# Performance work log

Hardware: AMD Instinct MI355X
Metric: run time of the kernel (lower is better)

## Reference

```python
import jax, jax.numpy as jnp
import numpy as np
from jax import lax

B, C, H, W = 16, 3, 64, 64
P = 256        # total_patches
PS = 9         # patch_size
E = 256        # attn_embed_dim
NH = 8         # attn_heads
POSD = 64      # pos_embed_dim
HW = H * W
DH = E // NH


def setup_inputs() -> dict:
    key = jax.random.key(0)
    ks = jax.random.split(key, 20)
    def rn(k, shape, fan_in):
        return jax.random.normal(k, shape, jnp.float32) * (1.0 / np.sqrt(fan_in))
    return {
        "x": jax.random.normal(ks[0], (B, C, H, W), jnp.float32),
        "conv_w": rn(ks[1], (P, C, PS, PS), C * PS * PS),
        "conv_b": jnp.zeros((P,), jnp.float32),
        "in_w": rn(ks[2], (HW, E), HW),
        "in_b": jnp.zeros((E,), jnp.float32),
        "wq": rn(ks[3], (E, E), E), "bq": jnp.zeros((E,), jnp.float32),
        "wk": rn(ks[4], (E, E), E), "bk": jnp.zeros((E,), jnp.float32),
        "wv": rn(ks[5], (E, E), E), "bv": jnp.zeros((E,), jnp.float32),
        "wo": rn(ks[6], (E, E), E), "bo": jnp.zeros((E,), jnp.float32),
        "out_w": rn(ks[7], (E, HW), E),
        "out_b": jnp.zeros((HW,), jnp.float32),
        "fc_w": rn(ks[8], (HW, 2), HW),
        "fc_b": jnp.zeros((2,), jnp.float32),
        "pos_w": rn(ks[9], (2, POSD), 2),
        "pos_b": jnp.zeros((POSD,), jnp.float32),
    }


# pixel-center normalized coords matching affine_grid(align_corners=False)
_BASE = (2.0 * jnp.arange(PS, dtype=jnp.float32) + 1.0) / PS - 1.0


def _sample_patch(img, tx, ty):
    # img: (C,H,W); tx, ty scalars. Replicates affine_grid + grid_sample
    # (bilinear, padding_mode='border', align_corners=False) WITHOUT the
    # full-image repeat of the original module.
    gx = (PS / W) * _BASE[None, :] + tx     # (PS,PS) x-coords
    gy = (PS / H) * _BASE[:, None] + ty     # (PS,PS) y-coords
    ix = ((gx + 1.0) * W - 1.0) * 0.5       # unnormalize, align_corners=False
    iy = ((gy + 1.0) * H - 1.0) * 0.5
    x0 = jnp.floor(ix); y0 = jnp.floor(iy)
    wx = ix - x0;       wy = iy - y0
    x0i = jnp.clip(x0.astype(jnp.int32), 0, W - 1)
    x1i = jnp.clip(x0.astype(jnp.int32) + 1, 0, W - 1)
    y0i = jnp.clip(y0.astype(jnp.int32), 0, H - 1)
    y1i = jnp.clip(y0.astype(jnp.int32) + 1, 0, H - 1)
    v00 = img[:, y0i, x0i]; v01 = img[:, y0i, x1i]
    v10 = img[:, y1i, x0i]; v11 = img[:, y1i, x1i]
    return (v00 * (1 - wx) * (1 - wy) + v01 * wx * (1 - wy)
            + v10 * (1 - wx) * wy + v11 * wx * wy)   # (C,PS,PS)


def _forward(x, conv_w, conv_b, in_w, in_b, wq, bq, wk, bk, wv, bv, wo, bo,
             out_w, out_b, fc_w, fc_b, pos_w, pos_b):
    # ConvBlock: conv (same padding for odd kernel) + ReLU
    feat = lax.conv_general_dilated(
        x, conv_w, (1, 1), [(PS // 2, PS // 2)] * 2,
        dimension_numbers=("NCHW", "OIHW", "NCHW"))
    feat = jax.nn.relu(feat + conv_b[None, :, None, None])   # (B,P,H,W)
    # ConvSelfAttn: tokens are the P channels, features are flattened HxW
    tok = feat.reshape(B, P, HW) @ in_w + in_b                # (B,P,E)
    q = (tok @ wq + bq).reshape(B, P, NH, DH)
    k = (tok @ wk + bk).reshape(B, P, NH, DH)
    v = (tok @ wv + bv).reshape(B, P, NH, DH)
    scores = jnp.einsum("bqhd,bkhd->bhqk", q, k) / np.sqrt(DH)
    attn = jax.nn.softmax(scores, axis=-1)
    o = jnp.einsum("bhqk,bkhd->bqhd", attn, v).reshape(B, P, E)
    o = o @ wo + bo
    feat2 = o @ out_w + out_b                                 # (B,P,HW)
    # translation params in [-1,1]
    tp = jnp.tanh(feat2 @ fc_w + fc_b)                        # (B,P,2)
    tx, ty = tp[..., 0], tp[..., 1]
    sample_bp = jax.vmap(jax.vmap(_sample_patch, in_axes=(None, 0, 0)),
                         in_axes=(0, 0, 0))
    patches = sample_bp(x, tx, ty)                            # (B,P,C,PS,PS)
    patches = patches.reshape(B, P, C * PS * PS)
    pos_embeds = tp @ pos_w + pos_b                           # (B,P,POSD)
    return patches, pos_embeds


def reference(x, conv_w, conv_b, in_w, in_b, wq, bq, wk, bk, wv, bv, wo, bo,
              out_w, out_b, fc_w, fc_b, pos_w, pos_b):
    return _forward(x, conv_w, conv_b, in_w, in_b, wq, bq, wk, bk, wv, bv,
                    wo, bo, out_w, out_b, fc_w, fc_b, pos_w, pos_b)
```

## Files before the change

### kernel.cpp

```cpp
#include <hip/hip_runtime.h>
#include <hip/hip_bf16.h>

#define Bd 16
#define Cd 3
#define Hd 64
#define Wd 64
#define Pd 256
#define PSd 9
#define Ed 256
#define NHd 8
#define DHd 32
#define HWd 4096
#define POSDd 64

typedef unsigned short u16;
typedef short short8 __attribute__((ext_vector_type(8)));
typedef float f32x4 __attribute__((ext_vector_type(4)));

__device__ __forceinline__ float bf2f(u16 u) {
    union { unsigned int i; float f; } c; c.i = ((unsigned int)u) << 16; return c.f;
}
__device__ __forceinline__ u16 f2bf(float f) {
    unsigned int x = __float_as_uint(f);
    unsigned int r = (x + 0x7fffu + ((x >> 16) & 1u)) >> 16;
    return (u16)r;
}

__global__ __launch_bounds__(64) void precompute_G(
    const float* __restrict__ out_w, const float* __restrict__ fc_w,
    const float* __restrict__ out_b, const float* __restrict__ fc_b,
    float* __restrict__ G, float* __restrict__ h0) {
    int blk = blockIdx.x, lane = threadIdx.x;
    if (blk < 256) {
        int e = blk;
        float a0 = 0.f, a1 = 0.f;
        for (int i = lane; i < HWd; i += 64) {
            float a = out_w[e * HWd + i];
            a0 += a * fc_w[2 * i];
            a1 += a * fc_w[2 * i + 1];
        }
        #pragma unroll
        for (int off = 32; off; off >>= 1) { a0 += __shfl_xor(a0, off); a1 += __shfl_xor(a1, off); }
        if (lane == 0) { G[2 * e] = a0; G[2 * e + 1] = a1; }
    } else {
        int j = blk - 256;
        float a = 0.f;
        for (int i = lane; i < HWd; i += 64) a += out_b[i] * fc_w[2 * i + j];
        #pragma unroll
        for (int off = 32; off; off >>= 1) a += __shfl_xor(a, off);
        if (lane == 0) h0[j] = a + fc_b[j];
    }
}

__global__ __launch_bounds__(64) void precompute_M2(
    const float* __restrict__ wo, const float* __restrict__ bo,
    const float* __restrict__ G, float* __restrict__ M2, float* __restrict__ h0) {
    int blk = blockIdx.x, lane = threadIdx.x;
    if (blk < 256) {
        float m0 = 0.f, m1 = 0.f;
        for (int f = lane; f < Ed; f += 64) {
            float wv = wo[blk * Ed + f];
            m0 += wv * G[2 * f];
            m1 += wv * G[2 * f + 1];
        }
        #pragma unroll
        for (int off = 32; off; off >>= 1) { m0 += __shfl_xor(m0, off); m1 += __shfl_xor(m1, off); }
        if (lane == 0) { M2[2 * blk] = m0; M2[2 * blk + 1] = m1; }
    } else {
        int j = blk - 256;
        float hh = 0.f;
        for (int f = lane; f < Ed; f += 64) hh += bo[f] * G[2 * f + j];
        #pragma unroll
        for (int off = 32; off; off >>= 1) hh += __shfl_xor(hh, off);
        if (lane == 0) h0[j] += hh;
    }
}

__global__ __launch_bounds__(256) void prep_weight_t(
    const float* __restrict__ W, u16* __restrict__ Th, u16* __restrict__ Tl,
    int K, int N) {
    __shared__ u16 th[64][65];
    __shared__ u16 tl[64][65];
    int k0 = blockIdx.x * 64, n0 = blockIdx.y * 64;
    int col = threadIdx.x & 63, r4 = threadIdx.x >> 6;
    #pragma unroll
    for (int i = 0; i < 16; i++) {
        int kr = 4 * i + r4;
        float v = W[(size_t)(k0 + kr) * N + n0 + col];
        u16 h = f2bf(v);
        th[col][kr] = h;
        tl[col][kr] = f2bf(v - bf2f(h));
    }
    __syncthreads();
    #pragma unroll
    for (int i = 0; i < 16; i++) {
        int nr = 4 * i + r4;
        Th[(size_t)(n0 + nr) * K + k0 + col] = th[nr][col];
        Tl[(size_t)(n0 + nr) * K + k0 + col] = tl[nr][col];
    }
}

__global__ __launch_bounds__(256) void prep_convw(
    const float* __restrict__ W, u16* __restrict__ Ah, u16* __restrict__ Al) {
    int p = blockIdx.x, k = threadIdx.x;
    float v = (k < 243) ? W[p * 243 + k] : 0.f;
    u16 h = f2bf(v);
    Ah[p * 256 + k] = h;
    Al[p * 256 + k] = f2bf(v - bf2f(h));
}

__global__ __launch_bounds__(256) void concat_bias(
    const float* __restrict__ bq, const float* __restrict__ bk,
    const float* __restrict__ bv, float* __restrict__ b3) {
    int t = threadIdx.x;
    b3[t] = bq[t]; b3[256 + t] = bk[t]; b3[512 + t] = bv[t];
}

__global__ __launch_bounds__(256, 2) void conv_gemm(
    const u16* __restrict__ Ah, const u16* __restrict__ Al,
    const float* __restrict__ x, const float* __restrict__ conv_b,
    u16* __restrict__ feat_hi, u16* __restrict__ feat_lo) {
    __shared__ u16 sBh[64 * 72], sBl[64 * 72];
    __shared__ float wls[3 * 9 * 72];
    int tid = threadIdx.x;
    int w = tid >> 6, L = tid & 63;
    int m16 = L & 15, qd = L >> 4;
    int y = blockIdx.x;
    int nb = y << 6;
    int b = blockIdx.y;

    for (int i = tid; i < 3 * 9 * 72; i += 256) wls[i] = 0.f;
    __syncthreads();
    for (int i = tid; i < 3 * 9 * 64; i += 256) {
        int c = i / 576, rem = i - c * 576, wr = rem >> 6, col = rem & 63;
        int iy = y - 4 + wr;
        if (iy >= 0 && iy < 64)
            wls[c * 648 + wr * 72 + 4 + col] = x[((b * 3 + c) << 12) + (iy << 6) + col];
    }
    __syncthreads();

    f32x4 acc[4][4];
    #pragma unroll
    for (int mt = 0; mt < 4; mt++)
        #pragma unroll
        for (int ct = 0; ct < 4; ct++) acc[mt][ct] = (f32x4){0.f, 0.f, 0.f, 0.f};

    int n = tid >> 2, kb = (tid & 3) << 4;
    int arow = w * 16 + m16;

    for (int k0 = 0; k0 < 256; k0 += 64) {
        short8 afh[4][2], afl[4][2];
        #pragma unroll
        for (int mt = 0; mt < 4; mt++)
            #pragma unroll
            for (int c = 0; c < 2; c++) {
                int ao = (mt * 64 + arow) * 256 + k0 + c * 32 + qd * 8;
                afh[mt][c] = *(const short8*)(Ah + ao);
                afl[mt][c] = *(const short8*)(Al + ao);
            }
        u16 hbuf[16] __attribute__((aligned(8)));
        u16 lbuf[16] __attribute__((aligned(8)));
        #pragma unroll
        for (int j = 0; j < 16; j++) {
            int k = k0 + kb + j;
            float v = 0.f;
            if (k < 243) {
                int c = (k >= 81) + (k >= 162);
                int rem = k - c * 81;
                int dy = (rem * 57) >> 9;
                int dx = rem - dy * 9;
                v = wls[c * 648 + dy * 72 + dx + n];
            }
            u16 h = f2bf(v);
            hbuf[j] = h;
            lbuf[j] = f2bf(v - bf2f(h));
        }
        __syncthreads();
        #pragma unroll
        for (int t = 0; t < 4; t++) {
            *(ushort4*)&sBh[n * 72 + kb + 4 * t] = *(ushort4*)&hbuf[4 * t];
            *(ushort4*)&sBl[n * 72 + kb + 4 * t] = *(ushort4*)&lbuf[4 * t];
        }
        __syncthreads();
        #pragma unroll
        for (int c = 0; c < 2; c++) {
            #pragma unroll
            for (int ct = 0; ct < 4; ct++) {
                int bb = (ct * 16 + m16) * 72 + c * 32 + qd * 8;
                short8 bH = *(const short8*)&sBh[bb];
                short8 bL = *(const short8*)&sBl[bb];
                #pragma unroll
                for (int mt = 0; mt < 4; mt++) {
                    acc[mt][ct] = __builtin_amdgcn_mfma_f32_16x16x32_bf16(afh[mt][c], bH, acc[mt][ct], 0, 0, 0);
                    acc[mt][ct] = __builtin_amdgcn_mfma_f32_16x16x32_bf16(afh[mt][c], bL, acc[mt][ct], 0, 0, 0);
                    acc[mt][ct] = __builtin_amdgcn_mfma_f32_16x16x32_bf16(afl[mt][c], bH, acc[mt][ct], 0, 0, 0);
                }
            }
        }
    }

    #pragma unroll
    for (int mt = 0; mt < 4; mt++) {
        #pragma unroll
        for (int i = 0; i < 4; i++) {
            int gr = mt * 64 + w * 16 + qd * 4 + i;
            float bv = conv_b[gr];
            #pragma unroll
            for (int ct = 0; ct < 4; ct++) {
                int gc = nb + ct * 16 + m16;
                float val = fmaxf(acc[mt][ct][i] + bv, 0.f);
                size_t oi = ((size_t)(b * 256 + gr)) * HWd + gc;
                u16 h = f2bf(val);
                feat_hi[oi] = h;
                feat_lo[oi] = f2bf(val - bf2f(h));
            }
        }
    }
}

__global__ __launch_bounds__(256, 4) void gemm_mfma3(
    const u16* __restrict__ Ah, const u16* __restrict__ Al,
    const u16* __restrict__ Bh, const u16* __restrict__ Bl,
    const float* __restrict__ bias,
    float* __restrict__ Co, u16* __restrict__ Ch, u16* __restrict__ Cl,
    int N, int K, int klen, long long pstride, int mode) {
    __shared__ u16 sAh[64 * 72], sAl[64 * 72], sBh[64 * 72], sBl[64 * 72];
    int tid = threadIdx.x;
    int w = tid >> 6;
    int L = tid & 63;
    int m16 = L & 15, qd = L >> 4;
    int mb = blockIdx.y * 64, nb = blockIdx.x * 64;
    int kbeg = blockIdx.z * klen;

    f32x4 acc[4];
    #pragma unroll
    for (int i = 0; i < 4; i++) acc[i] = (f32x4){0.f, 0.f, 0.f, 0.f};

    int r = tid >> 2, s = tid & 3;
    const u16* pAh = Ah + (size_t)(mb + r) * K + kbeg + s * 16;
    const u16* pAl = Al + (size_t)(mb + r) * K + kbeg + s * 16;
    const u16* pBh = Bh + (size_t)(nb + r) * K + kbeg + s * 16;
    const u16* pBl = Bl + (size_t)(nb + r) * K + kbeg + s * 16;
    u16* dAh = &sAh[r * 72 + s * 16];
    u16* dAl = &sAl[r * 72 + s * 16];
    u16* dBh = &sBh[r * 72 + s * 16];
    u16* dBl = &sBl[r * 72 + s * 16];

    uint4 a0 = *(const uint4*)(pAh);
    uint4 a1 = *(const uint4*)(pAh + 8);
    uint4 a2 = *(const uint4*)(pAl);
    uint4 a3 = *(const uint4*)(pAl + 8);
    uint4 b0 = *(const uint4*)(pBh);
    uint4 b1 = *(const uint4*)(pBh + 8);
    uint4 b2 = *(const uint4*)(pBl);
    uint4 b3 = *(const uint4*)(pBl + 8);

    for (int k0 = 0; k0 < klen; k0 += 64) {
        __syncthreads();
        *(uint4*)(dAh) = a0; *(uint4*)(dAh + 8) = a1;
        *(uint4*)(dAl) = a2; *(uint4*)(dAl + 8) = a3;
        *(uint4*)(dBh) = b0; *(uint4*)(dBh + 8) = b1;
        *(uint4*)(dBl) = b2; *(uint4*)(dBl + 8) = b3;
        __syncthreads();
        int kn = k0 + 64;
        if (kn < klen) {
            a0 = *(const uint4*)(pAh + kn);
            a1 = *(const uint4*)(pAh + kn + 8);
            a2 = *(const uint4*)(pAl + kn);
            a3 = *(const uint4*)(pAl + kn + 8);
            b0 = *(const uint4*)(pBh + kn);
            b1 = *(const uint4*)(pBh + kn + 8);
            b2 = *(const uint4*)(pBl + kn);
            b3 = *(const uint4*)(pBl + kn + 8);
        }
        #pragma unroll
        for (int c = 0; c < 2; c++) {
            int ab = (w * 16 + m16) * 72 + c * 32 + qd * 8;
            short8 aH = *(const short8*)&sAh[ab];
            short8 aL = *(const short8*)&sAl[ab];
            #pragma unroll
            for (int ct = 0; ct < 4; ct++) {
                int bb = (ct * 16 + m16) * 72 + c * 32 + qd * 8;
                short8 bH = *(const short8*)&sBh[bb];
                short8 bL = *(const short8*)&sBl[bb];
                acc[ct] = __builtin_amdgcn_mfma_f32_16x16x32_bf16(aH, bH, acc[ct], 0, 0, 0);
                acc[ct] = __builtin_amdgcn_mfma_f32_16x16x32_bf16(aH, bL, acc[ct], 0, 0, 0);
                acc[ct] = __builtin_amdgcn_mfma_f32_16x16x32_bf16(aL, bH, acc[ct], 0, 0, 0);
            }
        }
    }

    #pragma unroll
    for (int ct = 0; ct < 4; ct++) {
        int gc = nb + ct * 16 + m16;
        float bv = (mode == 2) ? 0.f : bias[gc];
        #pragma unroll
        for (int i = 0; i < 4; i++) {
            int gr = mb + w * 16 + qd * 4 + i;
            float val = acc[ct][i] + bv;
            size_t oi = (size_t)gr * N + gc;
            if (mode == 0) {
                Co[oi] = val;
            } else if (mode == 2) {
                Co[(size_t)blockIdx.z * pstride + oi] = val;
            } else {
                u16 h = f2bf(val);
                Ch[oi] = h;
                Cl[oi] = f2bf(val - bf2f(h));
            }
        }
    }
}

__global__ __launch_bounds__(256) void reduce_split(
    const float* __restrict__ part, const float* __restrict__ bias,
    u16* __restrict__ Ch, u16* __restrict__ Cl, int total) {
    int i = (blockIdx.x * 256 + threadIdx.x) * 4;
    if (i >= total) return;
    float4 s0 = *(const float4*)(part + i);
    float4 s1 = *(const float4*)(part + (size_t)total + i);
    float4 s2 = *(const float4*)(part + 2 * (size_t)total + i);
    float4 s3 = *(const float4*)(part + 3 * (size_t)total + i);
    float4 bv = *(const float4*)(bias + (i & 255));
    float v[4] = { s0.x + s1.x + s2.x + s3.x + bv.x,
                   s0.y + s1.y + s2.y + s3.y + bv.y,
                   s0.z + s1.z + s2.z + s3.z + bv.z,
                   s0.w + s1.w + s2.w + s3.w + bv.w };
    u16 hb[4] __attribute__((aligned(8)));
    u16 lb[4] __attribute__((aligned(8)));
    #pragma unroll
    for (int j = 0; j < 4; j++) {
        u16 h = f2bf(v[j]);
        hb[j] = h;
        lb[j] = f2bf(v[j] - bf2f(h));
    }
    *(ushort4*)(Ch + i) = *(ushort4*)hb;
    *(ushort4*)(Cl + i) = *(ushort4*)lb;
}

__global__ __launch_bounds__(256) void transpose_v(
    const u16* __restrict__ qkvh, const u16* __restrict__ qkvl,
    u16* __restrict__ vTh, u16* __restrict__ vTl) {
    __shared__ u16 th[32][264];
    __shared__ u16 tl[32][264];
    int b = blockIdx.x, h = blockIdx.y;
    int t = threadIdx.x;
    {
        const u16* srch = qkvh + ((size_t)(b * 256 + t)) * 768 + 512 + h * 32;
        const u16* srcl = qkvl + ((size_t)(b * 256 + t)) * 768 + 512 + h * 32;
        #pragma unroll
        for (int j = 0; j < 4; j++) {
            short8 vh = *(const short8*)(srch + j * 8);
            short8 vl = *(const short8*)(srcl + j * 8);
            #pragma unroll
            for (int e = 0; e < 8; e++) {
                th[j * 8 + e][t] = (u16)vh[e];
                tl[j * 8 + e][t] = (u16)vl[e];
            }
        }
    }
    __syncthreads();
    {
        int d = t >> 3, seg = t & 7;
        size_t dst = ((size_t)((b * 8 + h) * 32 + d)) * 256 + seg * 32;
        #pragma unroll
        for (int j = 0; j < 4; j++) {
            *(uint4*)(vTh + dst + j * 8) = *(uint4*)&th[d][seg * 32 + j * 8];
            *(uint4*)(vTl + dst + j * 8) = *(uint4*)&tl[d][seg * 32 + j * 8];
        }
    }
}

__global__ __launch_bounds__(256) void attention_mfma(
    const u16* __restrict__ qkvh, const u16* __restrict__ qkvl,
    const u16* __restrict__ vTh, const u16* __restrict__ vTl,
    float* __restrict__ o) {
    __shared__ u16 ph[4][16][264];
    int b = blockIdx.x, h = blockIdx.y, qc = blockIdx.z;
    int tid = threadIdx.x;
    int w = tid >> 6, L = tid & 63;
    int m16 = L & 15, qd = L >> 4;
    const float rs = 0.17677669529663687f;

    size_t qoff = ((size_t)(b * 256 + qc * 64 + w * 16 + m16)) * 768 + h * 32 + qd * 8;
    short8 qH = *(const short8*)(qkvh + qoff);
    short8 qL = *(const short8*)(qkvl + qoff);

    f32x4 sacc[16];
    #pragma unroll
    for (int nt = 0; nt < 16; nt++) {
        size_t koff = ((size_t)(b * 256 + nt * 16 + m16)) * 768 + 256 + h * 32 + qd * 8;
        short8 bH = *(const short8*)(qkvh + koff);
        short8 bL = *(const short8*)(qkvl + koff);
        f32x4 a = (f32x4){0.f, 0.f, 0.f, 0.f};
        a = __builtin_amdgcn_mfma_f32_16x16x32_bf16(qH, bH, a, 0, 0, 0);
        a = __builtin_amdgcn_mfma_f32_16x16x32_bf16(qH, bL, a, 0, 0, 0);
        a = __builtin_amdgcn_mfma_f32_16x16x32_bf16(qL, bH, a, 0, 0, 0);
        sacc[nt] = a;
    }

    float l4[4] = {0.f, 0.f, 0.f, 0.f};
    #pragma unroll
    for (int nt = 0; nt < 16; nt++)
        #pragma unroll
        for (int i = 0; i < 4; i++) {
            float p = __expf(sacc[nt][i] * rs);
            sacc[nt][i] = p;
            l4[i] += p;
        }
    #pragma unroll
    for (int i = 0; i < 4; i++) {
        l4[i] += __shfl_xor(l4[i], 1);
        l4[i] += __shfl_xor(l4[i], 2);
        l4[i] += __shfl_xor(l4[i], 4);
        l4[i] += __shfl_xor(l4[i], 8);
    }

    #pragma unroll
    for (int nt = 0; nt < 16; nt++)
        #pragma unroll
        for (int i = 0; i < 4; i++)
            ph[w][qd * 4 + i][nt * 16 + m16] = f2bf(sacc[nt][i]);

    f32x4 oacc[2];
    oacc[0] = (f32x4){0.f, 0.f, 0.f, 0.f};
    oacc[1] = (f32x4){0.f, 0.f, 0.f, 0.f};
    size_t vbase = ((size_t)(b * 8 + h)) * 32 * 256;
    #pragma unroll
    for (int kt = 0; kt < 8; kt++) {
        short8 pa = *(const short8*)&ph[w][m16][kt * 32 + qd * 8];
        #pragma unroll
        for (int ct = 0; ct < 2; ct++) {
            size_t voff = vbase + (size_t)(ct * 16 + m16) * 256 + kt * 32 + qd * 8;
            short8 vH = *(const short8*)(vTh + voff);
            short8 vL = *(const short8*)(vTl + voff);
            oacc[ct] = __builtin_amdgcn_mfma_f32_16x16x32_bf16(pa, vH, oacc[ct], 0, 0, 0);
            oacc[ct] = __builtin_amdgcn_mfma_f32_16x16x32_bf16(pa, vL, oacc[ct], 0, 0, 0);
        }
    }

    #pragma unroll
    for (int i = 0; i < 4; i++) {
        float rinv = 1.f / l4[i];
        int orow = b * 256 + qc * 64 + w * 16 + qd * 4 + i;
        #pragma unroll
        for (int ct = 0; ct < 2; ct++)
            o[(size_t)orow * 256 + h * 32 + ct * 16 + m16] = oacc[ct][i] * rinv;
    }
}

#define PATCH_OUT 995328
__global__ __launch_bounds__(256) void head_kernel(
    const float* __restrict__ o, const float* __restrict__ M2,
    const float* __restrict__ h0, const float* __restrict__ pos_w,
    const float* __restrict__ pos_b, const float* __restrict__ x,
    float* __restrict__ out) {
    int w = threadIdx.x >> 6, lane = threadIdx.x & 63;
    int bp = blockIdx.x * 4 + w;
    int b = bp >> 8;

    const float* orow = o + (size_t)bp * Ed;
    float4 o4 = *(const float4*)(orow + lane * 4);
    int e0 = lane * 4;
    float s0 = o4.x * M2[2 * e0 + 0] + o4.y * M2[2 * e0 + 2] + o4.z * M2[2 * e0 + 4] + o4.w * M2[2 * e0 + 6];
    float s1 = o4.x * M2[2 * e0 + 1] + o4.y * M2[2 * e0 + 3] + o4.z * M2[2 * e0 + 5] + o4.w * M2[2 * e0 + 7];
    #pragma unroll
    for (int off = 32; off; off >>= 1) { s0 += __shfl_xor(s0, off); s1 += __shfl_xor(s1, off); }

    float tx = tanhf(s0 + h0[0]);
    float ty = tanhf(s1 + h0[1]);

    {
        float pv = tx * pos_w[lane] + ty * pos_w[64 + lane] + pos_b[lane];
        out[PATCH_OUT + bp * POSDd + lane] = pv;
    }

    const float* xb = x + b * 3 * HWd;
    #pragma unroll
    for (int s = 0; s < 4; s++) {
        int idx = s * 64 + lane;
        if (idx < 243) {
            int c = idx / 81;
            int rem = idx - c * 81;
            int iy = rem / 9;
            int jx = rem - iy * 9;
            float basex = (2.f * jx + 1.f) / 9.f - 1.f;
            float basey = (2.f * iy + 1.f) / 9.f - 1.f;
            float gx = 0.140625f * basex + tx;
            float gy = 0.140625f * basey + ty;
            float ix  = ((gx + 1.f) * 64.f - 1.f) * 0.5f;
            float iyf = ((gy + 1.f) * 64.f - 1.f) * 0.5f;
            float x0f = floorf(ix), y0f = floorf(iyf);
            float wx = ix - x0f, wy = iyf - y0f;
            int x0i = min(max((int)x0f, 0), 63);
            int x1i = min(max((int)x0f + 1, 0), 63);
            int y0i = min(max((int)y0f, 0), 63);
            int y1i = min(max((int)y0f + 1, 0), 63);
            const float* xc = xb + c * HWd;
            float v00 = xc[y0i * Wd + x0i];
            float v01 = xc[y0i * Wd + x1i];
            float v10 = xc[y1i * Wd + x0i];
            float v11 = xc[y1i * Wd + x1i];
            float val = v00 * (1.f - wx) * (1.f - wy) + v01 * wx * (1.f - wy)
                      + v10 * (1.f - wx) * wy + v11 * wx * wy;
            out[bp * 243 + idx] = val;
        }
    }
}

extern "C" void kernel_launch(void* const* d_in, const int* in_sizes, int n_in,
                              void* d_out, int out_size, void* d_ws, size_t ws_size,
                              hipStream_t stream) {
    (void)in_sizes; (void)n_in; (void)out_size;
    const float* x      = (const float*)d_in[0];
    const float* conv_w = (const float*)d_in[1];
    const float* conv_b = (const float*)d_in[2];
    const float* in_w   = (const float*)d_in[3];
    const float* in_b   = (const float*)d_in[4];
    const float* wq     = (const float*)d_in[5];
    const float* bq     = (const float*)d_in[6];
    const float* wk     = (const float*)d_in[7];
    const float* bk     = (const float*)d_in[8];
    const float* wv     = (const float*)d_in[9];
    const float* bv     = (const float*)d_in[10];
    const float* wo     = (const float*)d_in[11];
    const float* bo     = (const float*)d_in[12];
    const float* out_w  = (const float*)d_in[13];
    const float* out_b  = (const float*)d_in[14];
    const float* fc_w   = (const float*)d_in[15];
    const float* fc_b   = (const float*)d_in[16];
    const float* pos_w  = (const float*)d_in[17];
    const float* pos_b  = (const float*)d_in[18];

    int CB = 16;
    for (;;) {
        size_t u16e = (size_t)(2 * CB + 4) * 1048576 + 2 * 196608 + 2 * 65536
                    + 2 * 3145728 + 2 * 1048576;
        size_t f32e = 768 + 1048576 + 4ull * CB * 65536 + 2048;
        if (u16e * 2 + f32e * 4 <= ws_size || CB == 1) break;
        CB >>= 1;
    }
    int nchunks = 16 / CB;

    char* base = (char*)d_ws;
    u16* feat_hi = (u16*)base;
    u16* feat_lo = feat_hi + (size_t)CB * 1048576;
    u16* tok_hi  = feat_lo + (size_t)CB * 1048576;
    u16* tok_lo  = tok_hi + 1048576;
    u16* inw_h   = tok_lo + 1048576;
    u16* inw_l   = inw_h + 1048576;
    u16* wqkv_h  = inw_l + 1048576;
    u16* wqkv_l  = wqkv_h + 196608;
    u16* convw_h = wqkv_l + 196608;
    u16* convw_l = convw_h + 65536;
    u16* qkvh    = convw_l + 65536;
    u16* qkvl    = qkvh + 3145728;
    u16* vTh     = qkvl + 3145728;
    u16* vTl     = vTh + 1048576;
    float* bqkv  = (float*)(vTl + 1048576);
    float* o     = bqkv + 768;
    float* part  = o + 1048576;
    float* G     = part + 4ull * CB * 65536;
    float* M2    = G + 512;
    float* h0    = M2 + 512;
    float* out   = (float*)d_out;

    hipLaunchKernelGGL(precompute_G, dim3(258), dim3(64), 0, stream,
                       out_w, fc_w, out_b, fc_b, G, h0);
    hipLaunchKernelGGL(precompute_M2, dim3(258), dim3(64), 0, stream,
                       wo, bo, G, M2, h0);
    hipLaunchKernelGGL(prep_weight_t, dim3(64, 4), dim3(256), 0, stream,
                       in_w, inw_h, inw_l, 4096, 256);
    hipLaunchKernelGGL(prep_weight_t, dim3(4, 4), dim3(256), 0, stream,
                       wq, wqkv_h, wqkv_l, 256, 256);
    hipLaunchKernelGGL(prep_weight_t, dim3(4, 4), dim3(256), 0, stream,
                       wk, wqkv_h + 256 * 256, wqkv_l + 256 * 256, 256, 256);
    hipLaunchKernelGGL(prep_weight_t, dim3(4, 4), dim3(256), 0, stream,
                       wv, wqkv_h + 512 * 256, wqkv_l + 512 * 256, 256, 256);
    hipLaunchKernelGGL(prep_convw, dim3(256), dim3(256), 0, stream,
                       conv_w, convw_h, convw_l);
    hipLaunchKernelGGL(concat_bias, dim3(1), dim3(256), 0, stream,
                       bq, bk, bv, bqkv);

    for (int c = 0; c < nchunks; ++c) {
        hipLaunchKernelGGL(conv_gemm, dim3(64, CB), dim3(256), 0, stream,
                           convw_h, convw_l,
                           x + (size_t)c * CB * 3 * HWd, conv_b,
                           feat_hi, feat_lo);
        hipLaunchKernelGGL(gemm_mfma3, dim3(4, CB * 4, 4), dim3(256), 0, stream,
                           feat_hi, feat_lo, inw_h, inw_l, in_b,
                           part, (u16*)nullptr, (u16*)nullptr,
                           256, 4096, 1024, (long long)CB * 65536, 2);
        hipLaunchKernelGGL(reduce_split, dim3(CB * 65536 / 1024), dim3(256), 0, stream,
                           part, in_b,
                           tok_hi + (size_t)c * CB * 65536,
                           tok_lo + (size_t)c * CB * 65536,
                           CB * 65536);
    }
    hipLaunchKernelGGL(gemm_mfma3, dim3(12, 64, 1), dim3(256), 0, stream,
                       tok_hi, tok_lo, wqkv_h, wqkv_l, bqkv,
                       (float*)nullptr, qkvh, qkvl, 768, 256, 256, 0LL, 1);
    hipLaunchKernelGGL(transpose_v, dim3(16, 8), dim3(256), 0, stream,
                       qkvh, qkvl, vTh, vTl);
    hipLaunchKernelGGL(attention_mfma, dim3(16, 8, 4), dim3(256), 0, stream,
                       qkvh, qkvl, vTh, vTl, o);
    hipLaunchKernelGGL(head_kernel, dim3(1024), dim3(256), 0, stream,
                       o, M2, h0, pos_w, pos_b, x, out);
}
```

Baseline: 270.7 us.

## Fuse weight-prep kernels into one launch and prefetch conv B-tile build

```diff
diff --git a/kernel.cpp b/kernel.cpp
--- a/kernel.cpp
+++ b/kernel.cpp
@@ -26,16 +26,61 @@
     return (u16)r;
 }
 
-__global__ __launch_bounds__(64) void precompute_G(
+__global__ __launch_bounds__(256) void prep_fused(
+    const float* __restrict__ conv_w, const float* __restrict__ in_w,
+    const float* __restrict__ wq, const float* __restrict__ wk,
+    const float* __restrict__ wv, const float* __restrict__ bq,
+    const float* __restrict__ bk, const float* __restrict__ bv,
     const float* __restrict__ out_w, const float* __restrict__ fc_w,
     const float* __restrict__ out_b, const float* __restrict__ fc_b,
-    float* __restrict__ G, float* __restrict__ h0) {
-    int blk = blockIdx.x, lane = threadIdx.x;
+    u16* __restrict__ convw_h, u16* __restrict__ convw_l,
+    u16* __restrict__ inw_h, u16* __restrict__ inw_l,
+    u16* __restrict__ wqkv_h, u16* __restrict__ wqkv_l,
+    float* __restrict__ bqkv, float* __restrict__ G, float* __restrict__ h0) {
+    __shared__ u16 th[64][65];
+    __shared__ u16 tl[64][65];
+    int blk = blockIdx.x, t = threadIdx.x;
+
     if (blk < 256) {
-        int e = blk;
+        float v = (t < 243) ? conv_w[blk * 243 + t] : 0.f;
+        u16 h = f2bf(v);
+        convw_h[blk * 256 + t] = h;
+        convw_l[blk * 256 + t] = f2bf(v - bf2f(h));
+    } else if (blk < 560) {
+        const float* W;
+        u16 *Th, *Tl;
+        int K, local;
+        if (blk < 272)      { W = wq;   Th = wqkv_h;              Tl = wqkv_l;              K = 256;  local = blk - 256; }
+        else if (blk < 288) { W = wk;   Th = wqkv_h + 256 * 256;  Tl = wqkv_l + 256 * 256;  K = 256;  local = blk - 272; }
+        else if (blk < 304) { W = wv;   Th = wqkv_h + 512 * 256;  Tl = wqkv_l + 512 * 256;  K = 256;  local = blk - 288; }
+        else                { W = in_w; Th = inw_h;               Tl = inw_l;               K = 4096; local = blk - 304; }
+        int kt = (K == 256) ? (local & 3) : (local & 63);
+        int nt = (K == 256) ? (local >> 2) : (local >> 6);
+        int k0 = kt * 64, n0 = nt * 64;
+        int col = t & 63, r4 = t >> 6;
+        #pragma unroll
+        for (int i = 0; i < 16; i++) {
+            int kr = 4 * i + r4;
+            float v = W[(size_t)(k0 + kr) * 256 + n0 + col];
+            u16 h = f2bf(v);
+            th[col][kr] = h;
+            tl[col][kr] = f2bf(v - bf2f(h));
+        }
+        __syncthreads();
+        #pragma unroll
+        for (int i = 0; i < 16; i++) {
+            int nr = 4 * i + r4;
+            Th[(size_t)(n0 + nr) * K + k0 + col] = th[nr][col];
+            Tl[(size_t)(n0 + nr) * K + k0 + col] = tl[nr][col];
+        }
+    } else if (blk == 560) {
+        bqkv[t] = bq[t]; bqkv[256 + t] = bk[t]; bqkv[512 + t] = bv[t];
+    } else if (blk < 625) {
+        int e = (blk - 561) * 4 + (t >> 6);
+        int lane = t & 63;
         float a0 = 0.f, a1 = 0.f;
         for (int i = lane; i < HWd; i += 64) {
-            float a = out_w[e * HWd + i];
+            float a = out_w[(size_t)e * HWd + i];
             a0 += a * fc_w[2 * i];
             a1 += a * fc_w[2 * i + 1];
         }
@@ -43,12 +88,14 @@
         for (int off = 32; off; off >>= 1) { a0 += __shfl_xor(a0, off); a1 += __shfl_xor(a1, off); }
         if (lane == 0) { G[2 * e] = a0; G[2 * e + 1] = a1; }
     } else {
-        int j = blk - 256;
-        float a = 0.f;
-        for (int i = lane; i < HWd; i += 64) a += out_b[i] * fc_w[2 * i + j];
-        #pragma unroll
-        for (int off = 32; off; off >>= 1) a += __shfl_xor(a, off);
-        if (lane == 0) h0[j] = a + fc_b[j];
+        int wj = t >> 6, lane = t & 63;
+        if (wj < 2) {
+            float a = 0.f;
+            for (int i = lane; i < HWd; i += 64) a += out_b[i] * fc_w[2 * i + wj];
+            #pragma unroll
+            for (int off = 32; off; off >>= 1) a += __shfl_xor(a, off);
+            if (lane == 0) h0[wj] = a + fc_b[wj];
+        }
     }
 }
 
@@ -76,47 +123,7 @@
     }
 }
 
-__global__ __launch_bounds__(256) void prep_weight_t(
-    const float* __restrict__ W, u16* __restrict__ Th, u16* __restrict__ Tl,
-    int K, int N) {
-    __shared__ u16 th[64][65];
-    __shared__ u16 tl[64][65];
-    int k0 = blockIdx.x * 64, n0 = blockIdx.y * 64;
-    int col = threadIdx.x & 63, r4 = threadIdx.x >> 6;
-    #pragma unroll
-    for (int i = 0; i < 16; i++) {
-        int kr = 4 * i + r4;
-        float v = W[(size_t)(k0 + kr) * N + n0 + col];
-        u16 h = f2bf(v);
-        th[col][kr] = h;
-        tl[col][kr] = f2bf(v - bf2f(h));
-    }
-    __syncthreads();
-    #pragma unroll
-    for (int i = 0; i < 16; i++) {
-        int nr = 4 * i + r4;
-        Th[(size_t)(n0 + nr) * K + k0 + col] = th[nr][col];
-        Tl[(size_t)(n0 + nr) * K + k0 + col] = tl[nr][col];
-    }
-}
-
-__global__ __launch_bounds__(256) void prep_convw(
-    const float* __restrict__ W, u16* __restrict__ Ah, u16* __restrict__ Al) {
-    int p = blockIdx.x, k = threadIdx.x;
-    float v = (k < 243) ? W[p * 243 + k] : 0.f;
-    u16 h = f2bf(v);
-    Ah[p * 256 + k] = h;
-    Al[p * 256 + k] = f2bf(v - bf2f(h));
-}
-
-__global__ __launch_bounds__(256) void concat_bias(
-    const float* __restrict__ bq, const float* __restrict__ bk,
-    const float* __restrict__ bv, float* __restrict__ b3) {
-    int t = threadIdx.x;
-    b3[t] = bq[t]; b3[256 + t] = bk[t]; b3[512 + t] = bv[t];
-}
-
-__global__ __launch_bounds__(256, 2) void conv_gemm(
+__global__ __launch_bounds__(256, 4) void conv_gemm(
     const u16* __restrict__ Ah, const u16* __restrict__ Al,
     const float* __restrict__ x, const float* __restrict__ conv_b,
     u16* __restrict__ feat_hi, u16* __restrict__ feat_lo) {
@@ -148,21 +155,12 @@
     int n = tid >> 2, kb = (tid & 3) << 4;
     int arow = w * 16 + m16;
 
-    for (int k0 = 0; k0 < 256; k0 += 64) {
-        short8 afh[4][2], afl[4][2];
-        #pragma unroll
-        for (int mt = 0; mt < 4; mt++)
-            #pragma unroll
-            for (int c = 0; c < 2; c++) {
-                int ao = (mt * 64 + arow) * 256 + k0 + c * 32 + qd * 8;
-                afh[mt][c] = *(const short8*)(Ah + ao);
-                afl[mt][c] = *(const short8*)(Al + ao);
-            }
-        u16 hbuf[16] __attribute__((aligned(8)));
-        u16 lbuf[16] __attribute__((aligned(8)));
+    u16 hbuf[16] __attribute__((aligned(8)));
+    u16 lbuf[16] __attribute__((aligned(8)));
+    auto build = [&](int kbase) {
         #pragma unroll
         for (int j = 0; j < 16; j++) {
-            int k = k0 + kb + j;
+            int k = kbase + kb + j;
             float v = 0.f;
             if (k < 243) {
                 int c = (k >= 81) + (k >= 162);
@@ -175,6 +173,19 @@
             hbuf[j] = h;
             lbuf[j] = f2bf(v - bf2f(h));
         }
+    };
+    build(0);
+
+    for (int k0 = 0; k0 < 256; k0 += 64) {
+        short8 afh[4][2], afl[4][2];
+        #pragma unroll
+        for (int mt = 0; mt < 4; mt++)
+            #pragma unroll
+            for (int c = 0; c < 2; c++) {
+                int ao = (mt * 64 + arow) * 256 + k0 + c * 32 + qd * 8;
+                afh[mt][c] = *(const short8*)(Ah + ao);
+                afl[mt][c] = *(const short8*)(Al + ao);
+            }
         __syncthreads();
         #pragma unroll
         for (int t = 0; t < 4; t++) {
@@ -182,6 +193,7 @@
             *(ushort4*)&sBl[n * 72 + kb + 4 * t] = *(ushort4*)&lbuf[4 * t];
         }
         __syncthreads();
+        if (k0 < 192) build(k0 + 64);
         #pragma unroll
         for (int c = 0; c < 2; c++) {
             #pragma unroll
@@ -565,22 +577,13 @@
     float* h0    = M2 + 512;
     float* out   = (float*)d_out;
 
-    hipLaunchKernelGGL(precompute_G, dim3(258), dim3(64), 0, stream,
-                       out_w, fc_w, out_b, fc_b, G, h0);
+    hipLaunchKernelGGL(prep_fused, dim3(626), dim3(256), 0, stream,
+                       conv_w, in_w, wq, wk, wv, bq, bk, bv,
+                       out_w, fc_w, out_b, fc_b,
+                       convw_h, convw_l, inw_h, inw_l,
+                       wqkv_h, wqkv_l, bqkv, G, h0);
     hipLaunchKernelGGL(precompute_M2, dim3(258), dim3(64), 0, stream,
                        wo, bo, G, M2, h0);
-    hipLaunchKernelGGL(prep_weight_t, dim3(64, 4), dim3(256), 0, stream,
-                       in_w, inw_h, inw_l, 4096, 256);
-    hipLaunchKernelGGL(prep_weight_t, dim3(4, 4), dim3(256), 0, stream,
-                       wq, wqkv_h, wqkv_l, 256, 256);
-    hipLaunchKernelGGL(prep_weight_t, dim3(4, 4), dim3(256), 0, stream,
-                       wk, wqkv_h + 256 * 256, wqkv_l + 256 * 256, 256, 256);
-    hipLaunchKernelGGL(prep_weight_t, dim3(4, 4), dim3(256), 0, stream,
-                       wv, wqkv_h + 512 * 256, wqkv_l + 512 * 256, 256, 256);
-    hipLaunchKernelGGL(prep_convw, dim3(256), dim3(256), 0, stream,
-                       conv_w, convw_h, convw_l);
-    hipLaunchKernelGGL(concat_bias, dim3(1), dim3(256), 0, stream,
-                       bq, bk, bv, bqkv);
 
     for (int c = 0; c < nchunks; ++c) {
         hipLaunchKernelGGL(conv_gemm, dim3(64, CB), dim3(256), 0, stream,
```

New measurement: 304.1 us. 1.12x slower.
